# Optimization experiments

Measured on AMD Instinct MI355X. Metric: run time of the kernel, lower is better.

## Reference

```python
import jax, jax.numpy as jnp
import numpy as np

D = 1024
H = 16
HD = D // H
S = 2048
B = 2
INNER = 4 * D
EPS = 1e-5


def _layernorm(x, w, b):
    mu = jnp.mean(x, axis=-1, keepdims=True)
    var = jnp.mean(jnp.square(x - mu), axis=-1, keepdims=True)
    return (x - mu) * jax.lax.rsqrt(var + EPS) * w + b


def _rope(x, cos, sin):
    # x: [B, S, H, HD]; cos/sin: [S, HD//2]
    xe, xo = x[..., 0::2], x[..., 1::2]
    c = cos[None, :, None, :]
    s = sin[None, :, None, :]
    oe = xe * c - xo * s
    oo = xe * s + xo * c
    return jnp.stack([oe, oo], axis=-1).reshape(x.shape)


def setup_inputs() -> dict:
    key = jax.random.key(0)
    ks = jax.random.split(key, 12)
    hidden_states = jax.random.normal(ks[0], (B, S, D), dtype=jnp.float32)
    time_step_emb = jax.random.normal(ks[1], (B, 6 * D), dtype=jnp.float32)
    # causal additive mask [1,1,S,S]
    causal = jnp.tril(jnp.ones((S, S), dtype=bool))
    attention_mask = jnp.where(causal, 0.0, -1e9).astype(jnp.float32)[None, None]
    # proper RoPE tables
    inv_freq = 1.0 / (10000.0 ** (np.arange(0, HD, 2, dtype=np.float32) / HD))
    t = np.arange(S, dtype=np.float32)
    freqs = np.outer(t, inv_freq)  # [S, HD//2]
    rope_cos = jnp.asarray(np.cos(freqs))
    rope_sin = jnp.asarray(np.sin(freqs))
    p = 0.02
    params = dict(
        ln1_w=jnp.ones((D,), jnp.float32), ln1_b=jnp.zeros((D,), jnp.float32),
        ln2_w=jnp.ones((D,), jnp.float32), ln2_b=jnp.zeros((D,), jnp.float32),
        c_attn_w=jax.random.normal(ks[2], (D, 3 * D), jnp.float32) * p,
        c_attn_b=jnp.zeros((3 * D,), jnp.float32),
        c_proj_w=jax.random.normal(ks[3], (D, D), jnp.float32) * p,
        c_proj_b=jnp.zeros((D,), jnp.float32),
        fc_w=jax.random.normal(ks[4], (D, INNER), jnp.float32) * p,
        fc_b=jnp.zeros((INNER,), jnp.float32),
        proj_w=jax.random.normal(ks[5], (INNER, D), jnp.float32) * p,
        proj_b=jnp.zeros((D,), jnp.float32),
        scale_shift_table=jax.random.normal(ks[6], (6, D), jnp.float32) / np.sqrt(D),
    )
    return dict(hidden_states=hidden_states, attention_mask=attention_mask,
                time_step_emb=time_step_emb, rope_cos=rope_cos, rope_sin=rope_sin,
                **params)


def reference(hidden_states, attention_mask, time_step_emb, rope_cos, rope_sin,
              ln1_w, ln1_b, ln2_w, ln2_b, c_attn_w, c_attn_b, c_proj_w, c_proj_b,
              fc_w, fc_b, proj_w, proj_b, scale_shift_table):
    b = hidden_states.shape[0]
    mods = scale_shift_table[None] + time_step_emb.reshape(b, 6, D)  # [B,6,D]
    sh_msa, sc_msa, g_msa, sh_mlp, sc_mlp, g_mlp = [mods[:, i:i + 1] for i in range(6)]

    residual = hidden_states
    h = _layernorm(hidden_states, ln1_w, ln1_b) * (1.0 + sc_msa) + sh_msa

    qkv = h @ c_attn_w + c_attn_b  # [B,S,3D]
    q, k, v = jnp.split(qkv, 3, axis=-1)
    q = _rope(q.reshape(b, S, H, HD), rope_cos, rope_sin)
    k = _rope(k.reshape(b, S, H, HD), rope_cos, rope_sin)
    v = v.reshape(b, S, H, HD)
    scores = jnp.einsum('bqhd,bkhd->bhqk', q, k) / np.sqrt(float(HD))
    scores = scores + attention_mask
    attn = jax.nn.softmax(scores, axis=-1)
    out = jnp.einsum('bhqk,bkhd->bqhd', attn, v).reshape(b, S, D)
    attn_out = out @ c_proj_w + c_proj_b

    hidden = attn_out * g_msa + residual
    residual = hidden
    h = _layernorm(hidden, ln2_w, ln2_b) * (1.0 + sc_mlp) + sh_mlp
    h = jax.nn.gelu(h @ fc_w + fc_b, approximate=True)  # gelu_new (tanh approx)
    h = h @ proj_w + proj_b
    return h * g_mlp + residual
```

## Files before the change

### kernel.cpp

```cpp
#include <hip/hip_runtime.h>
#include <hip/hip_bf16.h>

#define D_MODEL 1024
#define N_HEADS 16
#define HEAD_DIM 64
#define SEQ 2048
#define BATCH 2
#define INNER_DIM 4096
#define ROWS (BATCH*SEQ)

using f32x4  = __attribute__((ext_vector_type(4))) float;
using bf16x8 = __attribute__((ext_vector_type(8))) short;

__device__ __forceinline__ void gl_lds16(const void* g, void* l) {
  __builtin_amdgcn_global_load_lds(
      (const __attribute__((address_space(1))) void*)g,
      (__attribute__((address_space(3))) void*)l, 16, 0, 0);
}

__device__ __forceinline__ float bf2f(unsigned short u) {
  union { unsigned int i; float f; } v; v.i = ((unsigned int)u) << 16; return v.f;
}
__device__ __forceinline__ unsigned short f2bf(float f) {
  union { float f; unsigned int i; } v; v.f = f;
  unsigned int x = v.i;
  return (unsigned short)((x + 0x7fffu + ((x >> 16) & 1u)) >> 16);
}

__device__ __forceinline__ float exp2fast(float x) {
  return __builtin_amdgcn_exp2f(x);
}

__device__ __forceinline__ float gelu_tanh(float x) {
  float x3 = x * x * x;
  float z = 0.7978845608028654f * (x + 0.044715f * x3);
  z = fminf(z, 15.0f);
  float e = __expf(2.0f * z);
  float th = (e - 1.0f) / (e + 1.0f);
  return 0.5f * x * (1.0f + th);
}

__global__ void transpose_convert(const float* __restrict__ in,
                                  unsigned short* __restrict__ out,
                                  int K, int N) {
  __shared__ float tile[32][33];
  int n0 = blockIdx.x * 32, k0 = blockIdx.y * 32;
  int tx = threadIdx.x, ty = threadIdx.y;
#pragma unroll
  for (int i = 0; i < 4; i++)
    tile[ty + i * 8][tx] = in[(size_t)(k0 + ty + i * 8) * N + n0 + tx];
  __syncthreads();
#pragma unroll
  for (int i = 0; i < 4; i++)
    out[(size_t)(n0 + ty + i * 8) * K + k0 + tx] = f2bf(tile[tx][ty + i * 8]);
}

template<int SH_IDX, int SC_IDX>
__global__ void ln_mod_kernel(const float* __restrict__ x,
                              const float* __restrict__ lw,
                              const float* __restrict__ lb,
                              const float* __restrict__ sst,
                              const float* __restrict__ temb,
                              unsigned short* __restrict__ out) {
  int row = blockIdx.x;
  int b = row >> 11;
  int t = threadIdx.x;
  const float* xr = x + (size_t)row * D_MODEL;
  float4 v = ((const float4*)xr)[t];
  float s = v.x + v.y + v.z + v.w;
  float s2 = v.x * v.x + v.y * v.y + v.z * v.z + v.w * v.w;
#pragma unroll
  for (int o = 1; o < 64; o <<= 1) { s += __shfl_xor(s, o); s2 += __shfl_xor(s2, o); }
  __shared__ float red[8];
  int wid = t >> 6, lane = t & 63;
  if (lane == 0) { red[wid] = s; red[4 + wid] = s2; }
  __syncthreads();
  s = red[0] + red[1] + red[2] + red[3];
  s2 = red[4] + red[5] + red[6] + red[7];
  float mu = s * (1.0f / D_MODEL);
  float var = s2 * (1.0f / D_MODEL) - mu * mu;
  float rs = rsqrtf(var + 1e-5f);
  int d0 = t * 4;
  float xv[4] = { v.x, v.y, v.z, v.w };
  ushort4 ov;
  unsigned short* po = (unsigned short*)&ov;
#pragma unroll
  for (int j = 0; j < 4; j++) {
    int d = d0 + j;
    float ln = (xv[j] - mu) * rs * lw[d] + lb[d];
    float sc = sst[SC_IDX * D_MODEL + d] + temb[b * 6 * D_MODEL + SC_IDX * D_MODEL + d];
    float sh = sst[SH_IDX * D_MODEL + d] + temb[b * 6 * D_MODEL + SH_IDX * D_MODEL + d];
    po[j] = f2bf(ln * (1.0f + sc) + sh);
  }
  *((ushort4*)(out + (size_t)row * D_MODEL + d0)) = ov;
}

enum { EPI_QKV = 0, EPI_GELU = 2, EPI_PART = 3 };

template<int EPI, int BMF>
__global__ __launch_bounds__(256, 4)
void gemm_kernel(const unsigned short* __restrict__ A,
                 const unsigned short* __restrict__ Bt,
                 const float* __restrict__ bias,
                 void* C0, void* C1,
                 int N, int Ksub, int Kstride,
                 const float* __restrict__ cosb,
                 const float* __restrict__ sinb) {
  __shared__ unsigned short Alds[2][BMF * 32 * 32];
  __shared__ unsigned short Blds[2][128 * 32];
  const int t = threadIdx.x;
  const int w = t >> 6, l = t & 63;
  const int lg = l >> 4, ll = l & 15;
  const int wm = w >> 1, wn = w & 1;
  const int kbase = blockIdx.z * Ksub;

  const int nx = gridDim.x;
  const int nwg = nx * gridDim.y;
  const int lid = blockIdx.y * nx + blockIdx.x;
  const int nid = (lid & 7) * (nwg >> 3) + (lid >> 3);
  const int m0 = (nid / nx) * (BMF * 32), n0 = (nid % nx) * 128;

  void* Cout = blockIdx.z ? C1 : C0;

  f32x4 acc[BMF][4] = {};

  auto stage = [&](int k0, int buf) {
#pragma unroll
    for (int c = t; c < BMF * 128; c += 256) {
      int row = c >> 2, ch = c & 3;
      int chs = ch ^ ((row >> 1) & 3);
      gl_lds16(A + (size_t)(m0 + row) * Kstride + kbase + k0 + chs * 8,
               (char*)&Alds[buf][0] + c * 16);
    }
#pragma unroll
    for (int i = 0; i < 2; i++) {
      int c = i * 256 + t;
      int row = c >> 2, ch = c & 3;
      int chs = ch ^ ((row >> 1) & 3);
      gl_lds16(Bt + (size_t)(n0 + row) * Kstride + kbase + k0 + chs * 8,
               (char*)&Blds[buf][0] + c * 16);
    }
  };

  stage(0, 0);
  int buf = 0;
  const int nk = Ksub >> 5;
  for (int it = 0; it < nk; ++it) {
    if (it + 1 < nk) {
      stage((it + 1) * 32, buf ^ 1);
      if constexpr (BMF == 4) asm volatile("s_waitcnt vmcnt(4)" ::: "memory");
      else                    asm volatile("s_waitcnt vmcnt(3)" ::: "memory");
    } else {
      asm volatile("s_waitcnt vmcnt(0)" ::: "memory");
    }
    __builtin_amdgcn_s_barrier();
    asm volatile("" ::: "memory");

    bf16x8 af[BMF], bfr[4];
#pragma unroll
    for (int mf = 0; mf < BMF; mf++) {
      int row = wm * (BMF * 16) + mf * 16 + ll;
      int ch = lg ^ ((row >> 1) & 3);
      af[mf] = *(const bf16x8*)((const char*)&Alds[buf][0] + row * 64 + ch * 16);
    }
#pragma unroll
    for (int nf = 0; nf < 4; nf++) {
      int row = wn * 64 + nf * 16 + ll;
      int ch = lg ^ ((row >> 1) & 3);
      bfr[nf] = *(const bf16x8*)((const char*)&Blds[buf][0] + row * 64 + ch * 16);
    }
#pragma unroll
    for (int mf = 0; mf < BMF; mf++)
#pragma unroll
      for (int nf = 0; nf < 4; nf++)
        acc[mf][nf] = __builtin_amdgcn_mfma_f32_16x16x32_bf16(af[mf], bfr[nf], acc[mf][nf], 0, 0, 0);

    asm volatile("" ::: "memory");
    __builtin_amdgcn_s_barrier();
    buf ^= 1;
  }

#pragma unroll
  for (int mf = 0; mf < BMF; mf++) {
#pragma unroll
    for (int nf = 0; nf < 4; nf++) {
      int col = n0 + wn * 64 + nf * 16 + ll;
      float bv = (EPI == EPI_PART) ? 0.0f : bias[col];
#pragma unroll
      for (int r = 0; r < 4; r++) {
        int row = m0 + wm * (BMF * 16) + mf * 16 + lg * 4 + r;
        float v = acc[mf][nf][r] + bv;
        if constexpr (EPI == EPI_QKV) {
          if (col < 2048) {
            float vp = __shfl_xor(v, 1);
            int sp = row & (SEQ - 1);
            int ip = (col & 63) >> 1;
            float cz = cosb[sp * 32 + ip], sz = sinb[sp * 32 + ip];
            float ov = (col & 1) ? (vp * sz + v * cz) : (v * cz - vp * sz);
            if (col < 1024) ov *= 0.18033688011112042f;
            v = ov;
          }
          ((unsigned short*)Cout)[(size_t)row * N + col] = f2bf(v);
        } else if constexpr (EPI == EPI_GELU) {
          ((unsigned short*)Cout)[(size_t)row * N + col] = f2bf(gelu_tanh(v));
        } else {
          ((unsigned short*)Cout)[(size_t)row * N + col] = f2bf(v);
        }
      }
    }
  }
}

__global__ void reduce_gated(const unsigned short* __restrict__ p0,
                             const unsigned short* __restrict__ p1,
                             const float* __restrict__ bias,
                             const float* __restrict__ sst,
                             const float* __restrict__ temb,
                             int g_idx,
                             const float* __restrict__ resid,
                             float* __restrict__ out) {
  int i = blockIdx.x * 256 + threadIdx.x;
  int idx = i * 4;
  int col = idx & 1023;
  int b = idx >> 21;
  ushort4 a0 = *(const ushort4*)(p0 + idx);
  ushort4 a1 = *(const ushort4*)(p1 + idx);
  float4 rv = *(const float4*)(resid + idx);
  float4 o;
  const unsigned short* s0 = (const unsigned short*)&a0;
  const unsigned short* s1 = (const unsigned short*)&a1;
  float* po = (float*)&o;
  const float* pr = (const float*)&rv;
#pragma unroll
  for (int j = 0; j < 4; j++) {
    float s = bf2f(s0[j]) + bf2f(s1[j]) + bias[col + j];
    float g = sst[g_idx * D_MODEL + col + j] + temb[b * 6 * D_MODEL + g_idx * D_MODEL + col + j];
    po[j] = s * g + pr[j];
  }
  *(float4*)(out + idx) = o;
}

__global__ __launch_bounds__(256, 4)
void attn_kernel(const unsigned short* __restrict__ qkv,
                 unsigned short* __restrict__ attn_o) {
  __shared__ unsigned short Klds[2][64 * 64];
  __shared__ unsigned short Vt[2][64 * 64];
  __shared__ unsigned short Plds[4][16 * 64];

  const int id = blockIdx.x;
  const int bh = id & 31;
  const int b = bh >> 4, h = bh & 15;
  const int q0 = (31 - (id >> 5)) * 64;
  const int t = threadIdx.x;
  const int w = t >> 6, l = t & 63;
  const int lg = l >> 4, ll = l & 15;
  const int qw0 = q0 + w * 16;
  const int q_lane = qw0 + ll;

  bf16x8 qf[2];
  {
    const unsigned short* qb = qkv + (size_t)(b * SEQ + q_lane) * 3072 + h * 64;
    qf[0] = *(const bf16x8*)(qb + lg * 8);
    qf[1] = *(const bf16x8*)(qb + 32 + lg * 8);
  }

  const int kp = t & 31, dg = t >> 5;

  f32x4 oacc[4] = {};
  float mrun = -1e30f, lrun = 0.0f;

  {
#pragma unroll
    for (int i = 0; i < 2; i++) {
      int c = i * 256 + t;
      int kr = c >> 3, cc = c & 7;
      gl_lds16(qkv + (size_t)(b * SEQ + kr) * 3072 + 1024 + h * 64 + (cc ^ (kr & 7)) * 8,
               (char*)&Klds[0][0] + c * 16);
    }
    const unsigned short* vp = qkv + (size_t)(b * SEQ + 2 * kp) * 3072 + 2048 + h * 64 + dg * 8;
    union { uint4 u; unsigned short s[8]; } a0, a1;
    a0.u = *(const uint4*)vp;
    a1.u = *(const uint4*)(vp + 3072);
    unsigned int* vt32 = (unsigned int*)&Vt[0][0];
#pragma unroll
    for (int i = 0; i < 8; i++)
      vt32[(dg * 8 + i) * 32 + (((kp >> 2) ^ i) << 2) + (kp & 3)] =
          (unsigned int)a0.s[i] | ((unsigned int)a1.s[i] << 16);
  }
  __syncthreads();

  int buf = 0;
  for (int k0 = 0; k0 <= q0; k0 += 64) {
    const bool has_next = (k0 + 64 <= q0);
    union { uint4 u; unsigned short s[8]; } n0, n1;
    if (has_next) {
#pragma unroll
      for (int i = 0; i < 2; i++) {
        int c = i * 256 + t;
        int kr = c >> 3, cc = c & 7;
        gl_lds16(qkv + (size_t)(b * SEQ + k0 + 64 + kr) * 3072 + 1024 + h * 64 + (cc ^ (kr & 7)) * 8,
                 (char*)&Klds[buf ^ 1][0] + c * 16);
      }
      const unsigned short* vp =
          qkv + (size_t)(b * SEQ + k0 + 64 + 2 * kp) * 3072 + 2048 + h * 64 + dg * 8;
      n0.u = *(const uint4*)vp;
      n1.u = *(const uint4*)(vp + 3072);
    }

    f32x4 s[4] = {};
#pragma unroll
    for (int kk = 0; kk < 2; kk++) {
#pragma unroll
      for (int nf = 0; nf < 4; nf++) {
        int key = nf * 16 + ll;
        int cc = (kk * 4 + lg) ^ (key & 7);
        bf16x8 kf = *(const bf16x8*)((const char*)&Klds[buf][0] + key * 128 + cc * 16);
        s[nf] = __builtin_amdgcn_mfma_f32_16x16x32_bf16(kf, qf[kk], s[nf], 0, 0, 0);
      }
    }
    if (k0 == q0) {
#pragma unroll
      for (int nf = 0; nf < 4; nf++) {
        int key = k0 + nf * 16 + lg * 4;
#pragma unroll
        for (int r = 0; r < 4; r++)
          if (key + r > q_lane) s[nf][r] = -1e30f;
      }
    }
    float mx = -1e30f;
#pragma unroll
    for (int nf = 0; nf < 4; nf++)
#pragma unroll
      for (int r = 0; r < 4; r++) mx = fmaxf(mx, s[nf][r]);
    mx = fmaxf(mx, __shfl_xor(mx, 16));
    mx = fmaxf(mx, __shfl_xor(mx, 32));
    float mnew = fmaxf(mrun, mx);
    float alpha = exp2fast(mrun - mnew);
    mrun = mnew;
    float ps = 0.0f;
#pragma unroll
    for (int nf = 0; nf < 4; nf++)
#pragma unroll
      for (int r = 0; r < 4; r++) {
        float p = exp2fast(s[nf][r] - mnew);
        s[nf][r] = p;
        ps += p;
      }
    ps += __shfl_xor(ps, 16);
    ps += __shfl_xor(ps, 32);
    lrun = lrun * alpha + ps;
#pragma unroll
    for (int nf = 0; nf < 4; nf++)
#pragma unroll
      for (int r = 0; r < 4; r++) oacc[nf][r] *= alpha;

#pragma unroll
    for (int nf = 0; nf < 4; nf++) {
      unsigned int lo = (unsigned int)f2bf(s[nf][0]) | ((unsigned int)f2bf(s[nf][1]) << 16);
      unsigned int hi = (unsigned int)f2bf(s[nf][2]) | ((unsigned int)f2bf(s[nf][3]) << 16);
      int chunk = (nf * 2 + (lg >> 1)) ^ (ll & 7);
      uint2 pv; pv.x = lo; pv.y = hi;
      *(uint2*)((char*)&Plds[w][0] + ll * 128 + chunk * 16 + (lg & 1) * 8) = pv;
    }
    bf16x8 pb[2];
#pragma unroll
    for (int kk = 0; kk < 2; kk++) {
      int pc = (kk * 4 + lg) ^ (ll & 7);
      pb[kk] = *(const bf16x8*)((char*)&Plds[w][0] + ll * 128 + pc * 16);
    }
#pragma unroll
    for (int nf = 0; nf < 4; nf++) {
      int d = nf * 16 + ll;
#pragma unroll
      for (int kk = 0; kk < 2; kk++) {
        int vc = (kk * 4 + lg) ^ (d & 7);
        bf16x8 vb = *(const bf16x8*)((const char*)&Vt[buf][0] + d * 128 + vc * 16);
        oacc[nf] = __builtin_amdgcn_mfma_f32_16x16x32_bf16(vb, pb[kk], oacc[nf], 0, 0, 0);
      }
    }
    if (has_next) {
      unsigned int* vt32 = (unsigned int*)&Vt[buf ^ 1][0];
#pragma unroll
      for (int i = 0; i < 8; i++)
        vt32[(dg * 8 + i) * 32 + (((kp >> 2) ^ i) << 2) + (kp & 3)] =
            (unsigned int)n0.s[i] | ((unsigned int)n1.s[i] << 16);
    }
    __syncthreads();
    buf ^= 1;
  }

  float rl = 1.0f / lrun;
#pragma unroll
  for (int nf = 0; nf < 4; nf++) {
    ushort4 ov;
    ov.x = f2bf(oacc[nf][0] * rl);
    ov.y = f2bf(oacc[nf][1] * rl);
    ov.z = f2bf(oacc[nf][2] * rl);
    ov.w = f2bf(oacc[nf][3] * rl);
    *(ushort4*)(attn_o + (size_t)(b * SEQ + q_lane) * D_MODEL + h * 64 + nf * 16 + lg * 4) = ov;
  }
}

extern "C" void kernel_launch(void* const* d_in, const int* in_sizes, int n_in,
                              void* d_out, int out_size, void* d_ws, size_t ws_size,
                              hipStream_t stream) {
  const float* hidden_states = (const float*)d_in[0];
  const float* temb     = (const float*)d_in[2];
  const float* rope_cos = (const float*)d_in[3];
  const float* rope_sin = (const float*)d_in[4];
  const float* ln1_w    = (const float*)d_in[5];
  const float* ln1_b    = (const float*)d_in[6];
  const float* ln2_w    = (const float*)d_in[7];
  const float* ln2_b    = (const float*)d_in[8];
  const float* c_attn_w = (const float*)d_in[9];
  const float* c_attn_b = (const float*)d_in[10];
  const float* c_proj_w = (const float*)d_in[11];
  const float* c_proj_b = (const float*)d_in[12];
  const float* fc_w     = (const float*)d_in[13];
  const float* fc_b     = (const float*)d_in[14];
  const float* proj_w   = (const float*)d_in[15];
  const float* proj_b   = (const float*)d_in[16];
  const float* sst      = (const float*)d_in[17];

  char* ws = (char*)d_ws;
  unsigned short* wqkv  = (unsigned short*)(ws + 0);
  unsigned short* wproj = (unsigned short*)(ws + 6291456);
  unsigned short* wfc   = (unsigned short*)(ws + 8388608);
  unsigned short* wp2   = (unsigned short*)(ws + 16777216);
  unsigned short* hln   = (unsigned short*)(ws + 25165824);
  unsigned short* qkvb  = (unsigned short*)(ws + 33554432);
  unsigned short* attno = (unsigned short*)(ws + 58720256);
  float*          hidden = (float*)(ws + 67108864);
  unsigned short* rp0 = (unsigned short*)(ws + 33554432);
  unsigned short* rp1 = (unsigned short*)(ws + 41943040);
  unsigned short* h3  = (unsigned short*)(ws + 33554432);
  unsigned short* fp0 = (unsigned short*)(ws + 0);
  unsigned short* fp1 = (unsigned short*)(ws + 8388608);

  dim3 tb(32, 8);
  transpose_convert<<<dim3(3072 / 32, 1024 / 32), tb, 0, stream>>>(c_attn_w, wqkv, 1024, 3072);
  transpose_convert<<<dim3(1024 / 32, 1024 / 32), tb, 0, stream>>>(c_proj_w, wproj, 1024, 1024);
  transpose_convert<<<dim3(4096 / 32, 1024 / 32), tb, 0, stream>>>(fc_w, wfc, 1024, 4096);
  transpose_convert<<<dim3(1024 / 32, 4096 / 32), tb, 0, stream>>>(proj_w, wp2, 4096, 1024);

  ln_mod_kernel<0, 1><<<ROWS, 256, 0, stream>>>(hidden_states, ln1_w, ln1_b, sst, temb, hln);

  gemm_kernel<EPI_QKV, 2><<<dim3(3072 / 128, ROWS / 64, 1), 256, 0, stream>>>(
      hln, wqkv, c_attn_b, qkvb, qkvb, 3072, 1024, 1024, rope_cos, rope_sin);

  attn_kernel<<<dim3(32 * 32), 256, 0, stream>>>(qkvb, attno);

  gemm_kernel<EPI_PART, 2><<<dim3(1024 / 128, ROWS / 64, 2), 256, 0, stream>>>(
      attno, wproj, c_proj_b, rp0, rp1, 1024, 512, 1024, nullptr, nullptr);
  reduce_gated<<<(ROWS * D_MODEL / 4) / 256, 256, 0, stream>>>(
      rp0, rp1, c_proj_b, sst, temb, 2, hidden_states, hidden);

  ln_mod_kernel<3, 4><<<ROWS, 256, 0, stream>>>(hidden, ln2_w, ln2_b, sst, temb, hln);

  gemm_kernel<EPI_GELU, 2><<<dim3(4096 / 128, ROWS / 64, 1), 256, 0, stream>>>(
      hln, wfc, fc_b, h3, h3, 4096, 1024, 1024, nullptr, nullptr);

  gemm_kernel<EPI_PART, 2><<<dim3(1024 / 128, ROWS / 64, 2), 256, 0, stream>>>(
      h3, wp2, proj_b, fp0, fp1, 1024, 2048, 4096, nullptr, nullptr);
  reduce_gated<<<(ROWS * D_MODEL / 4) / 256, 256, 0, stream>>>(
      fp0, fp1, proj_b, sst, temb, 5, hidden, (float*)d_out);
}
```

Measured before the change: 293.5 us.

## Enlarge GEMM tiles to 128x128 with 64-wide K steps

Replaces the 64x128 GEMM tile (K step 32) with a 128x128 tile and a K step of 64. Each wave now computes a 4x4 grid of MFMA fragments across two k-substeps, and the LDS swizzle changes to an 8-chunk XOR pattern. The larger tile raises arithmetic intensity and halves the number of barriers per K. In exchange it uses more LDS (64KB double-buffered) and more registers, so occupancy is capped at 2 blocks per CU and fewer workgroups are launched. That risks under-filling the 256 CUs for the N=1024 GEMMs.

```diff
diff --git a/kernel.cpp b/kernel.cpp
--- a/kernel.cpp
+++ b/kernel.cpp
@@ -97,17 +97,17 @@
 
 enum { EPI_QKV = 0, EPI_GELU = 2, EPI_PART = 3 };
 
-template<int EPI, int BMF>
-__global__ __launch_bounds__(256, 4)
-void gemm_kernel(const unsigned short* __restrict__ A,
-                 const unsigned short* __restrict__ Bt,
-                 const float* __restrict__ bias,
-                 void* C0, void* C1,
-                 int N, int Ksub, int Kstride,
-                 const float* __restrict__ cosb,
-                 const float* __restrict__ sinb) {
-  __shared__ unsigned short Alds[2][BMF * 32 * 32];
-  __shared__ unsigned short Blds[2][128 * 32];
+template<int EPI>
+__global__ __launch_bounds__(256, 2)
+void gemm64(const unsigned short* __restrict__ A,
+            const unsigned short* __restrict__ Bt,
+            const float* __restrict__ bias,
+            void* C0, void* C1,
+            int N, int Ksub, int Kstride,
+            const float* __restrict__ cosb,
+            const float* __restrict__ sinb) {
+  __shared__ unsigned short Alds[2][128 * 64];
+  __shared__ unsigned short Blds[2][128 * 64];
   const int t = threadIdx.x;
   const int w = t >> 6, l = t & 63;
   const int lg = l >> 4, ll = l & 15;
@@ -118,62 +118,63 @@
   const int nwg = nx * gridDim.y;
   const int lid = blockIdx.y * nx + blockIdx.x;
   const int nid = (lid & 7) * (nwg >> 3) + (lid >> 3);
-  const int m0 = (nid / nx) * (BMF * 32), n0 = (nid % nx) * 128;
+  const int m0 = (nid / nx) * 128, n0 = (nid % nx) * 128;
 
   void* Cout = blockIdx.z ? C1 : C0;
 
-  f32x4 acc[BMF][4] = {};
-
-  auto stage = [&](int k0, int buf) {
-#pragma unroll
-    for (int c = t; c < BMF * 128; c += 256) {
-      int row = c >> 2, ch = c & 3;
-      int chs = ch ^ ((row >> 1) & 3);
-      gl_lds16(A + (size_t)(m0 + row) * Kstride + kbase + k0 + chs * 8,
+  f32x4 acc[4][4] = {};
+
+  auto stage = [&](int kt, int buf) {
+#pragma unroll
+    for (int i = 0; i < 4; i++) {
+      int c = i * 256 + t;
+      int row = c >> 3, q = c & 7;
+      gl_lds16(A + (size_t)(m0 + row) * Kstride + kbase + kt * 64 + ((q ^ (row & 7)) << 3),
                (char*)&Alds[buf][0] + c * 16);
     }
 #pragma unroll
-    for (int i = 0; i < 2; i++) {
+    for (int i = 0; i < 4; i++) {
       int c = i * 256 + t;
-      int row = c >> 2, ch = c & 3;
-      int chs = ch ^ ((row >> 1) & 3);
-      gl_lds16(Bt + (size_t)(n0 + row) * Kstride + kbase + k0 + chs * 8,
+      int row = c >> 3, q = c & 7;
+      gl_lds16(Bt + (size_t)(n0 + row) * Kstride + kbase + kt * 64 + ((q ^ (row & 7)) << 3),
                (char*)&Blds[buf][0] + c * 16);
     }
   };
 
   stage(0, 0);
   int buf = 0;
-  const int nk = Ksub >> 5;
+  const int nk = Ksub >> 6;
   for (int it = 0; it < nk; ++it) {
     if (it + 1 < nk) {
-      stage((it + 1) * 32, buf ^ 1);
-      if constexpr (BMF == 4) asm volatile("s_waitcnt vmcnt(4)" ::: "memory");
-      else                    asm volatile("s_waitcnt vmcnt(3)" ::: "memory");
+      stage(it + 1, buf ^ 1);
+      asm volatile("s_waitcnt vmcnt(8)" ::: "memory");
     } else {
       asm volatile("s_waitcnt vmcnt(0)" ::: "memory");
     }
     __builtin_amdgcn_s_barrier();
     asm volatile("" ::: "memory");
 
-    bf16x8 af[BMF], bfr[4];
-#pragma unroll
-    for (int mf = 0; mf < BMF; mf++) {
-      int row = wm * (BMF * 16) + mf * 16 + ll;
-      int ch = lg ^ ((row >> 1) & 3);
-      af[mf] = *(const bf16x8*)((const char*)&Alds[buf][0] + row * 64 + ch * 16);
-    }
-#pragma unroll
-    for (int nf = 0; nf < 4; nf++) {
-      int row = wn * 64 + nf * 16 + ll;
-      int ch = lg ^ ((row >> 1) & 3);
-      bfr[nf] = *(const bf16x8*)((const char*)&Blds[buf][0] + row * 64 + ch * 16);
-    }
-#pragma unroll
-    for (int mf = 0; mf < BMF; mf++)
-#pragma unroll
-      for (int nf = 0; nf < 4; nf++)
-        acc[mf][nf] = __builtin_amdgcn_mfma_f32_16x16x32_bf16(af[mf], bfr[nf], acc[mf][nf], 0, 0, 0);
+#pragma unroll
+    for (int kk = 0; kk < 2; kk++) {
+      bf16x8 af[4], bfr[4];
+#pragma unroll
+      for (int mf = 0; mf < 4; mf++) {
+        int row = wm * 64 + mf * 16 + ll;
+        int q = (kk * 4 + lg) ^ (row & 7);
+        af[mf] = *(const bf16x8*)(&Alds[buf][0] + row * 64 + q * 8);
+      }
+#pragma unroll
+      for (int nf = 0; nf < 4; nf++) {
+        int row = wn * 64 + nf * 16 + ll;
+        int q = (kk * 4 + lg) ^ (row & 7);
+        bfr[nf] = *(const bf16x8*)(&Blds[buf][0] + row * 64 + q * 8);
+      }
+#pragma unroll
+      for (int mf = 0; mf < 4; mf++)
+#pragma unroll
+        for (int nf = 0; nf < 4; nf++)
+          acc[mf][nf] = __builtin_amdgcn_mfma_f32_16x16x32_bf16(af[mf], bfr[nf], acc[mf][nf], 0, 0, 0);
+    }
 
     asm volatile("" ::: "memory");
     __builtin_amdgcn_s_barrier();
@@ -181,14 +182,14 @@
   }
 
 #pragma unroll
-  for (int mf = 0; mf < BMF; mf++) {
+  for (int mf = 0; mf < 4; mf++) {
 #pragma unroll
     for (int nf = 0; nf < 4; nf++) {
       int col = n0 + wn * 64 + nf * 16 + ll;
       float bv = (EPI == EPI_PART) ? 0.0f : bias[col];
 #pragma unroll
       for (int r = 0; r < 4; r++) {
-        int row = m0 + wm * (BMF * 16) + mf * 16 + lg * 4 + r;
+        int row = m0 + wm * 64 + mf * 16 + lg * 4 + r;
         float v = acc[mf][nf][r] + bv;
         if constexpr (EPI == EPI_QKV) {
           if (col < 2048) {
@@ -445,22 +446,22 @@
 
   ln_mod_kernel<0, 1><<<ROWS, 256, 0, stream>>>(hidden_states, ln1_w, ln1_b, sst, temb, hln);
 
-  gemm_kernel<EPI_QKV, 2><<<dim3(3072 / 128, ROWS / 64, 1), 256, 0, stream>>>(
+  gemm64<EPI_QKV><<<dim3(3072 / 128, ROWS / 128, 1), 256, 0, stream>>>(
       hln, wqkv, c_attn_b, qkvb, qkvb, 3072, 1024, 1024, rope_cos, rope_sin);
 
   attn_kernel<<<dim3(32 * 32), 256, 0, stream>>>(qkvb, attno);
 
-  gemm_kernel<EPI_PART, 2><<<dim3(1024 / 128, ROWS / 64, 2), 256, 0, stream>>>(
+  gemm64<EPI_PART><<<dim3(1024 / 128, ROWS / 128, 2), 256, 0, stream>>>(
       attno, wproj, c_proj_b, rp0, rp1, 1024, 512, 1024, nullptr, nullptr);
   reduce_gated<<<(ROWS * D_MODEL / 4) / 256, 256, 0, stream>>>(
       rp0, rp1, c_proj_b, sst, temb, 2, hidden_states, hidden);
 
   ln_mod_kernel<3, 4><<<ROWS, 256, 0, stream>>>(hidden, ln2_w, ln2_b, sst, temb, hln);
 
-  gemm_kernel<EPI_GELU, 2><<<dim3(4096 / 128, ROWS / 64, 1), 256, 0, stream>>>(
+  gemm64<EPI_GELU><<<dim3(4096 / 128, ROWS / 128, 1), 256, 0, stream>>>(
       hln, wfc, fc_b, h3, h3, 4096, 1024, 1024, nullptr, nullptr);
 
-  gemm_kernel<EPI_PART, 2><<<dim3(1024 / 128, ROWS / 64, 2), 256, 0, stream>>>(
+  gemm64<EPI_PART><<<dim3(1024 / 128, ROWS / 128, 2), 256, 0, stream>>>(
       h3, wp2, proj_b, fp0, fp1, 1024, 2048, 4096, nullptr, nullptr);
   reduce_gated<<<(ROWS * D_MODEL / 4) / 256, 256, 0, stream>>>(
       fp0, fp1, proj_b, sst, temb, 5, hidden, (float*)d_out);
```

After: 268.6 us. 1.09x faster.
